# Kernel optimization log

Measured on AMD Instinct MI355X. Metric: run time of the kernel, lower is better.

Reference implementation:

```python
import jax, jax.numpy as jnp
import numpy as np

N_USERS = 200000
N_ITEMS = 100000
EMB_DIM = 64
N_LAYERS = 4
E_POS = 2000000
E_NEG = 500000


def _propagate(row, col, user_emb, item_emb, edge_weight, n_users, n_items):
    # LightGCN-style symmetric degree-normalized neighbor aggregation.
    deg_u = jnp.clip(jnp.zeros((n_users,), jnp.float32).at[row].add(1.0), 1.0)
    deg_i = jnp.clip(jnp.zeros((n_items,), jnp.float32).at[col].add(1.0), 1.0)
    norm = jax.lax.rsqrt(deg_u)[row] * jax.lax.rsqrt(deg_i)[col] * edge_weight  # [E]
    # gather -> scale -> scatter_add, both directions
    item_to_user = jnp.zeros_like(user_emb).at[row].add(item_emb[col] * norm[:, None])
    user_to_item = jnp.zeros_like(item_emb).at[col].add(user_emb[row] * norm[:, None])
    return user_emb + item_to_user, item_emb + user_to_item


def setup_inputs() -> dict:
    key = jax.random.key(0)
    k1, k2, k3, k4, k5, k6 = jax.random.split(key, 6)
    # Xavier-normal-ish init: std = sqrt(2/(fan_in+fan_out))
    std_u = np.sqrt(2.0 / (N_USERS + EMB_DIM)).astype(np.float32)
    std_i = np.sqrt(2.0 / (N_ITEMS + EMB_DIM)).astype(np.float32)
    return {
        "edge_index": jax.random.randint(k1, (2, E_POS), 0, N_ITEMS, dtype=jnp.int32),
        "negative_edge_index": jax.random.randint(k2, (2, E_NEG), 0, N_ITEMS, dtype=jnp.int32),
        "edge_weight": jnp.ones((E_POS,), jnp.float32),
        "user_emb_pos_w": jax.random.normal(k3, (N_USERS, EMB_DIM), jnp.float32) * std_u,
        "item_emb_pos_w": jax.random.normal(k4, (N_ITEMS, EMB_DIM), jnp.float32) * std_i,
        "user_emb_neg_w": jax.random.normal(k5, (N_USERS, EMB_DIM), jnp.float32) * std_u,
        "item_emb_neg_w": jax.random.normal(k6, (N_ITEMS, EMB_DIM), jnp.float32) * std_i,
    }


def reference(edge_index, negative_edge_index, edge_weight,
              user_emb_pos_w, item_emb_pos_w, user_emb_neg_w, item_emb_neg_w):
    row, col = edge_index[0], edge_index[1]
    nrow, ncol = negative_edge_index[0], negative_edge_index[1]
    neg_w = jnp.ones_like(nrow, dtype=jnp.float32)

    ue_p, ie_p = user_emb_pos_w, item_emb_pos_w
    ue_n, ie_n = user_emb_neg_w, item_emb_neg_w
    sum_up, sum_ip = ue_p, ie_p
    sum_un, sum_in = ue_n, ie_n
    for _ in range(N_LAYERS):
        ue_p, ie_p = _propagate(row, col, ue_p, ie_p, edge_weight, N_USERS, N_ITEMS)
        sum_up = sum_up + ue_p
        sum_ip = sum_ip + ie_p
    for _ in range(N_LAYERS):
        ue_n, ie_n = _propagate(nrow, ncol, ue_n, ie_n, neg_w, N_USERS, N_ITEMS)
        sum_un = sum_un + ue_n
        sum_in = sum_in + ie_n
    inv = 1.0 / (N_LAYERS + 1)
    return (sum_up * inv, sum_ip * inv, sum_un * inv, sum_in * inv)
```

## Files before the change

### kernel.cpp

```cpp
#include <hip/hip_runtime.h>
#include <hip/hip_fp16.h>

#define DIM 64
#define CHUNK 2048


__global__ void hist_kernel(const int* __restrict__ row, const int* __restrict__ col,
                            int* __restrict__ deg, int NU, int E) {
    int e = blockIdx.x * blockDim.x + threadIdx.x;
    if (e < E) {
        atomicAdd(&deg[row[e]], 1);
        atomicAdd(&deg[NU + col[e]], 1);
    }
}

__global__ void fill_rsqrt(const int* __restrict__ deg, float* __restrict__ r, int n) {
    int i = blockIdx.x * blockDim.x + threadIdx.x;
    if (i < n) r[i] = rsqrtf(fmaxf((float)deg[i], 1.0f));
}

__global__ void partial_sums(const int* __restrict__ deg, int* __restrict__ bsum, int n) {
    __shared__ int s[256];
    int t = threadIdx.x;
    int base = blockIdx.x * CHUNK + t * 8;
    int loc = 0;
    for (int k = 0; k < 8; k++) { int j = base + k; if (j < n) loc += deg[j]; }
    s[t] = loc; __syncthreads();
    for (int ofs = 128; ofs > 0; ofs >>= 1) { if (t < ofs) s[t] += s[t + ofs]; __syncthreads(); }
    if (t == 0) bsum[blockIdx.x] = s[0];
}

__global__ void scan_block(int* __restrict__ bsum, int nb) {
    __shared__ int s[256];
    int t = threadIdx.x;
    int x = (t < nb) ? bsum[t] : 0;
    s[t] = x; __syncthreads();
    for (int ofs = 1; ofs < 256; ofs <<= 1) {
        int y = (t >= ofs) ? s[t - ofs] : 0;
        __syncthreads();
        s[t] += y;
        __syncthreads();
    }
    if (t < nb) bsum[t] = s[t] - x;
}

__global__ void scan_chunk(const int* __restrict__ deg, int* __restrict__ offs,
                           int* __restrict__ cur, const int* __restrict__ bsum, int n) {
    __shared__ int s[256];
    int t = threadIdx.x;
    int base = blockIdx.x * CHUNK + t * 8;
    int v[8]; int loc = 0;
    for (int k = 0; k < 8; k++) { int j = base + k; v[k] = (j < n) ? deg[j] : 0; loc += v[k]; }
    s[t] = loc; __syncthreads();
    for (int ofs = 1; ofs < 256; ofs <<= 1) {
        int x = (t >= ofs) ? s[t - ofs] : 0;
        __syncthreads();
        s[t] += x;
        __syncthreads();
    }
    int excl = (t == 0) ? 0 : s[t - 1];
    int run = bsum[blockIdx.x] + excl;
    for (int k = 0; k < 8; k++) {
        int j = base + k;
        if (j < n) { offs[j] = run; cur[j] = run; }
        run += v[k];
    }
}

__global__ void scatter_kernel(const int* __restrict__ row, const int* __restrict__ col,
                               const float* __restrict__ w, int has_w,
                               const float* __restrict__ rs,
                               int* __restrict__ cur, int2* __restrict__ adj,
                               int NU, int E) {
    int e = blockIdx.x * blockDim.x + threadIdx.x;
    if (e >= E) return;
    int r = row[e], c = col[e];
    float wv = has_w ? w[e] : 1.0f;
    float nrm = rs[r] * rs[NU + c] * wv;
    int nb = __float_as_int(nrm);
    int pu = atomicAdd(&cur[r], 1);
    adj[pu] = make_int2(c, nb);
    int pi = atomicAdd(&cur[NU + c], 1);
    adj[pi] = make_int2(r, nb);
}


__global__ void init3(const float* __restrict__ src, float* __restrict__ cur,
                      float* __restrict__ sum, uint2* __restrict__ h, int n4) {
    int i = blockIdx.x * blockDim.x + threadIdx.x;
    if (i < n4) {
        float4 v = ((const float4*)src)[i];
        ((float4*)cur)[i] = v;
        ((float4*)sum)[i] = v;
        __half2 a = __floats2half2_rn(v.x, v.y);
        __half2 b = __floats2half2_rn(v.z, v.w);
        uint2 u; u.x = *(unsigned*)&a; u.y = *(unsigned*)&b;
        h[i] = u;
    }
}

__global__ void aggregate(const int* __restrict__ offs, const int* __restrict__ endo,
                          const int2* __restrict__ adj,
                          const uint2* __restrict__ src_h,
                          const float* __restrict__ self_old,
                          float* __restrict__ self_new,
                          uint2* __restrict__ self_h,
                          float* __restrict__ sum,
                          float scale, int wh, int N) {
    int v = blockIdx.x * (blockDim.x >> 6) + (threadIdx.x >> 6);
    if (v >= N) return;
    v = __builtin_amdgcn_readfirstlane(v);
    int s = offs[v], e = endo[v];
    if (s == e) return;
    int l = threadIdx.x & 63;
    int q = l >> 4;
    int c = l & 15;

    float ax = 0.f, ay = 0.f, az = 0.f, aw = 0.f;
    for (int i = s; i < e; i += 8) {
        int i0 = i + q;
        int i1 = i + 4 + q;
        int2 m0 = adj[min(i0, e - 1)];
        int2 m1 = adj[min(i1, e - 1)];
        float w0 = (i0 < e) ? __int_as_float(m0.y) : 0.0f;
        float w1 = (i1 < e) ? __int_as_float(m1.y) : 0.0f;
        uint2 h0 = src_h[(size_t)m0.x * 16 + c];
        uint2 h1 = src_h[(size_t)m1.x * 16 + c];
        float2 f00 = __half22float2(*(__half2*)&h0.x);
        float2 f01 = __half22float2(*(__half2*)&h0.y);
        float2 f10 = __half22float2(*(__half2*)&h1.x);
        float2 f11 = __half22float2(*(__half2*)&h1.y);
        ax += f00.x * w0; ay += f00.y * w0; az += f01.x * w0; aw += f01.y * w0;
        ax += f10.x * w1; ay += f10.y * w1; az += f11.x * w1; aw += f11.y * w1;
    }
    ax += __shfl_xor(ax, 16); ay += __shfl_xor(ay, 16);
    az += __shfl_xor(az, 16); aw += __shfl_xor(aw, 16);
    ax += __shfl_xor(ax, 32); ay += __shfl_xor(ay, 32);
    az += __shfl_xor(az, 32); aw += __shfl_xor(aw, 32);

    if (q == 0) {
        size_t ro4 = (size_t)v * (DIM / 4) + c;
        float4 so = ((const float4*)self_old)[ro4];
        float4 fin;
        fin.x = so.x + ax; fin.y = so.y + ay; fin.z = so.z + az; fin.w = so.w + aw;
        ((float4*)self_new)[ro4] = fin;
        if (wh) {
            __half2 hA = __floats2half2_rn(fin.x, fin.y);
            __half2 hB = __floats2half2_rn(fin.z, fin.w);
            uint2 hw2; hw2.x = *(unsigned*)&hA; hw2.y = *(unsigned*)&hB;
            self_h[ro4] = hw2;
        }
        float4 sm = ((const float4*)sum)[ro4];
        sm.x = (sm.x + fin.x) * scale; sm.y = (sm.y + fin.y) * scale;
        sm.z = (sm.z + fin.z) * scale; sm.w = (sm.w + fin.w) * scale;
        ((float4*)sum)[ro4] = sm;
    }
}


static inline int cdiv(long long a, int b) { return (int)((a + b - 1) / b); }

extern "C" void kernel_launch(void* const* d_in, const int* in_sizes, int n_in,
                              void* d_out, int out_size, void* d_ws, size_t ws_size,
                              hipStream_t stream) {
    const int*   ei  = (const int*)d_in[0];
    const int*   nei = (const int*)d_in[1];
    const float* ew  = (const float*)d_in[2];
    const float* uep = (const float*)d_in[3];
    const float* iep = (const float*)d_in[4];
    const float* uen = (const float*)d_in[5];
    const float* ien = (const float*)d_in[6];
    float* out = (float*)d_out;

    const int E_POS = in_sizes[2];
    const int E_NEG = in_sizes[1] / 2;
    const int NU = in_sizes[3] / DIM;
    const int NI = in_sizes[4] / DIM;
    const int NV = NU + NI;
    const int NTOT = NV * DIM;

    char* ws = (char*)d_ws;
    size_t off = 0;
    auto alloc = [&](size_t elems4) { void* p = ws + off; off += elems4 * 4; return p; };
    float* u_emb  = (float*)alloc((size_t)NU * DIM);
    float* i_emb0 = (float*)alloc((size_t)NI * DIM);
    float* i_emb1 = (float*)alloc((size_t)NI * DIM);
    uint2* u_h    = (uint2*)alloc((size_t)NU * DIM / 2);
    uint2* i_h0   = (uint2*)alloc((size_t)NI * DIM / 2);
    uint2* i_h1   = (uint2*)alloc((size_t)NI * DIM / 2);
    int*   offs = (int*)alloc(NV);
    int*   cur  = (int*)alloc(NV);
    float* rs   = (float*)alloc(NV);
    int*   bsum = (int*)alloc(256);
    int2*  adj  = (int2*)alloc((size_t)E_POS * 2);

    const int B = 256;
    const int nb = cdiv(NV, CHUNK);

    for (int g = 0; g < 2; ++g) {
        const int    E   = g == 0 ? E_POS : E_NEG;
        const int*   row = g == 0 ? ei : nei;
        const int*   col = row + E;
        const float* wv  = g == 0 ? ew : nullptr;
        const float* ue0 = g == 0 ? uep : uen;
        const float* ie0 = g == 0 ? iep : ien;
        float* sum_u = out + (size_t)g * NTOT;
        float* sum_i = sum_u + (size_t)NU * DIM;

        hipMemsetAsync(cur, 0, (size_t)NV * sizeof(int), stream);
        hist_kernel<<<cdiv(E, B), B, 0, stream>>>(row, col, cur, NU, E);
        fill_rsqrt<<<cdiv(NV, B), B, 0, stream>>>(cur, rs, NV);
        partial_sums<<<nb, B, 0, stream>>>(cur, bsum, NV);
        scan_block<<<1, 256, 0, stream>>>(bsum, nb);
        scan_chunk<<<nb, B, 0, stream>>>(cur, offs, cur, bsum, NV);
        scatter_kernel<<<cdiv(E, B), B, 0, stream>>>(row, col, wv, g == 0 ? 1 : 0,
                                                     rs, cur, adj, NU, E);

        init3<<<cdiv(NU * DIM / 4, B), B, 0, stream>>>(ue0, u_emb, sum_u, u_h, NU * DIM / 4);
        init3<<<cdiv(NI * DIM / 4, B), B, 0, stream>>>(ie0, i_emb0, sum_i, i_h0, NI * DIM / 4);

        float* icur = i_emb0;
        float* inew = i_emb1;
        uint2* ihcur = i_h0;
        uint2* ihnew = i_h1;
        for (int l = 0; l < 4; ++l) {
            float scale = (l == 3) ? 0.2f : 1.0f;
            int wh = (l == 3) ? 0 : 1;
            aggregate<<<cdiv(NI, 4), B, 0, stream>>>(
                offs + NU, cur + NU, adj, u_h, icur, inew, ihnew, sum_i, scale, wh, NI);
            aggregate<<<cdiv(NU, 4), B, 0, stream>>>(
                offs, cur, adj, ihcur, u_emb, u_emb, u_h, sum_u, scale, wh, NU);
            float* t = icur; icur = inew; inew = t;
            uint2* th = ihcur; ihcur = ihnew; ihnew = th;
        }
    }
}
```

Baseline: 1.634 ms.

## Merge user/item aggregation into one launch and keep layer state in fp16

Each layer now runs one aggregate launch over all user and item vertices instead of two. Each thread picks its source, self and destination buffers by checking whether the vertex is a user or an item. The fp32 current-embedding buffers are removed: the self term is read from the fp16 copy, and users get double-buffered fp16 state. This cuts per-layer reads and writes and halves launch count. The trade-off is a small precision loss, because the self term is now rounded to fp16 every layer. The adjacency allocation is also enlarged to match its real size.

```diff
diff --git a/kernel.cpp b/kernel.cpp
--- a/kernel.cpp
+++ b/kernel.cpp
@@ -85,12 +85,11 @@
 }
 
 
-__global__ void init3(const float* __restrict__ src, float* __restrict__ cur,
-                      float* __restrict__ sum, uint2* __restrict__ h, int n4) {
+__global__ void init_h(const float* __restrict__ src, float* __restrict__ sum,
+                       uint2* __restrict__ h, int n4) {
     int i = blockIdx.x * blockDim.x + threadIdx.x;
     if (i < n4) {
         float4 v = ((const float4*)src)[i];
-        ((float4*)cur)[i] = v;
         ((float4*)sum)[i] = v;
         __half2 a = __floats2half2_rn(v.x, v.y);
         __half2 b = __floats2half2_rn(v.z, v.w);
@@ -101,17 +100,26 @@
 
 __global__ void aggregate(const int* __restrict__ offs, const int* __restrict__ endo,
                           const int2* __restrict__ adj,
-                          const uint2* __restrict__ src_h,
-                          const float* __restrict__ self_old,
-                          float* __restrict__ self_new,
-                          uint2* __restrict__ self_h,
-                          float* __restrict__ sum,
-                          float scale, int wh, int N) {
+                          const uint2* __restrict__ u_cur,
+                          const uint2* __restrict__ i_cur,
+                          uint2* __restrict__ u_new,
+                          uint2* __restrict__ i_new,
+                          float* __restrict__ sum_u,
+                          float* __restrict__ sum_i,
+                          float scale, int wh, int NU, int NV) {
     int v = blockIdx.x * (blockDim.x >> 6) + (threadIdx.x >> 6);
-    if (v >= N) return;
+    if (v >= NV) return;
     v = __builtin_amdgcn_readfirstlane(v);
     int s = offs[v], e = endo[v];
     if (s == e) return;
+
+    bool isU = v < NU;
+    const uint2* src   = isU ? i_cur : u_cur;
+    const uint2* selfT = isU ? u_cur : i_cur;
+    uint2*       dstT  = isU ? u_new : i_new;
+    float*       sum   = isU ? sum_u : sum_i;
+    int vl = isU ? v : v - NU;
+
     int l = threadIdx.x & 63;
     int q = l >> 4;
     int c = l & 15;
@@ -124,8 +132,8 @@
         int2 m1 = adj[min(i1, e - 1)];
         float w0 = (i0 < e) ? __int_as_float(m0.y) : 0.0f;
         float w1 = (i1 < e) ? __int_as_float(m1.y) : 0.0f;
-        uint2 h0 = src_h[(size_t)m0.x * 16 + c];
-        uint2 h1 = src_h[(size_t)m1.x * 16 + c];
+        uint2 h0 = src[(size_t)m0.x * 16 + c];
+        uint2 h1 = src[(size_t)m1.x * 16 + c];
         float2 f00 = __half22float2(*(__half2*)&h0.x);
         float2 f01 = __half22float2(*(__half2*)&h0.y);
         float2 f10 = __half22float2(*(__half2*)&h1.x);
@@ -139,21 +147,22 @@
     az += __shfl_xor(az, 32); aw += __shfl_xor(aw, 32);
 
     if (q == 0) {
-        size_t ro4 = (size_t)v * (DIM / 4) + c;
-        float4 so = ((const float4*)self_old)[ro4];
+        size_t ro = (size_t)vl * 16 + c;
+        uint2 hs = selfT[ro];
+        float2 s01 = __half22float2(*(__half2*)&hs.x);
+        float2 s23 = __half22float2(*(__half2*)&hs.y);
         float4 fin;
-        fin.x = so.x + ax; fin.y = so.y + ay; fin.z = so.z + az; fin.w = so.w + aw;
-        ((float4*)self_new)[ro4] = fin;
+        fin.x = s01.x + ax; fin.y = s01.y + ay; fin.z = s23.x + az; fin.w = s23.y + aw;
         if (wh) {
             __half2 hA = __floats2half2_rn(fin.x, fin.y);
             __half2 hB = __floats2half2_rn(fin.z, fin.w);
             uint2 hw2; hw2.x = *(unsigned*)&hA; hw2.y = *(unsigned*)&hB;
-            self_h[ro4] = hw2;
+            dstT[ro] = hw2;
         }
-        float4 sm = ((const float4*)sum)[ro4];
+        float4 sm = ((const float4*)sum)[ro];
         sm.x = (sm.x + fin.x) * scale; sm.y = (sm.y + fin.y) * scale;
         sm.z = (sm.z + fin.z) * scale; sm.w = (sm.w + fin.w) * scale;
-        ((float4*)sum)[ro4] = sm;
+        ((float4*)sum)[ro] = sm;
     }
 }
 
@@ -182,17 +191,15 @@
     char* ws = (char*)d_ws;
     size_t off = 0;
     auto alloc = [&](size_t elems4) { void* p = ws + off; off += elems4 * 4; return p; };
-    float* u_emb  = (float*)alloc((size_t)NU * DIM);
-    float* i_emb0 = (float*)alloc((size_t)NI * DIM);
-    float* i_emb1 = (float*)alloc((size_t)NI * DIM);
-    uint2* u_h    = (uint2*)alloc((size_t)NU * DIM / 2);
-    uint2* i_h0   = (uint2*)alloc((size_t)NI * DIM / 2);
-    uint2* i_h1   = (uint2*)alloc((size_t)NI * DIM / 2);
+    uint2* u_h0 = (uint2*)alloc((size_t)NU * DIM / 2);
+    uint2* u_h1 = (uint2*)alloc((size_t)NU * DIM / 2);
+    uint2* i_h0 = (uint2*)alloc((size_t)NI * DIM / 2);
+    uint2* i_h1 = (uint2*)alloc((size_t)NI * DIM / 2);
     int*   offs = (int*)alloc(NV);
     int*   cur  = (int*)alloc(NV);
     float* rs   = (float*)alloc(NV);
     int*   bsum = (int*)alloc(256);
-    int2*  adj  = (int2*)alloc((size_t)E_POS * 2);
+    int2*  adj  = (int2*)alloc((size_t)E_POS * 4);
 
     const int B = 256;
     const int nb = cdiv(NV, CHUNK);
@@ -216,22 +223,20 @@
         scatter_kernel<<<cdiv(E, B), B, 0, stream>>>(row, col, wv, g == 0 ? 1 : 0,
                                                      rs, cur, adj, NU, E);
 
-        init3<<<cdiv(NU * DIM / 4, B), B, 0, stream>>>(ue0, u_emb, sum_u, u_h, NU * DIM / 4);
-        init3<<<cdiv(NI * DIM / 4, B), B, 0, stream>>>(ie0, i_emb0, sum_i, i_h0, NI * DIM / 4);
-
-        float* icur = i_emb0;
-        float* inew = i_emb1;
-        uint2* ihcur = i_h0;
-        uint2* ihnew = i_h1;
+        init_h<<<cdiv(NU * DIM / 4, B), B, 0, stream>>>(ue0, sum_u, u_h0, NU * DIM / 4);
+        init_h<<<cdiv(NI * DIM / 4, B), B, 0, stream>>>(ie0, sum_i, i_h0, NI * DIM / 4);
+
+        uint2* ucur = u_h0; uint2* unew = u_h1;
+        uint2* icur = i_h0; uint2* inew = i_h1;
         for (int l = 0; l < 4; ++l) {
             float scale = (l == 3) ? 0.2f : 1.0f;
             int wh = (l == 3) ? 0 : 1;
-            aggregate<<<cdiv(NI, 4), B, 0, stream>>>(
-                offs + NU, cur + NU, adj, u_h, icur, inew, ihnew, sum_i, scale, wh, NI);
-            aggregate<<<cdiv(NU, 4), B, 0, stream>>>(
-                offs, cur, adj, ihcur, u_emb, u_emb, u_h, sum_u, scale, wh, NU);
-            float* t = icur; icur = inew; inew = t;
-            uint2* th = ihcur; ihcur = ihnew; ihnew = th;
+            aggregate<<<cdiv(NV, 4), B, 0, stream>>>(
+                offs, cur, adj, ucur, icur, unew, inew, sum_u, sum_i,
+                scale, wh, NU, NV);
+            uint2* t;
+            t = ucur; ucur = unew; unew = t;
+            t = icur; icur = inew; inew = t;
         }
     }
 }
```

Result: faster. 1.545 ms (-5.5%).
